# Optimization experiments

Measured on AMD Instinct MI355X. Metric: run time of the kernel, lower is better.

## Reference

```python
import jax, jax.numpy as jnp
import numpy as np


def setup_inputs() -> dict:
    key = jax.random.key(0)
    k1, k2 = jax.random.split(key)
    N, M, Q, D = 4096, 128, 64, 128
    a_embeddings = jax.random.normal(k1, (N, D), dtype=jnp.float32)
    b_embedding_sets = jax.random.normal(k2, (M, Q, D), dtype=jnp.float32)
    gaussian_variance = jnp.full((1,), 0.5, dtype=jnp.float32)  # nn.Parameter default
    return {
        "a_embeddings": a_embeddings,
        "b_embedding_sets": b_embedding_sets,
        "gaussian_variance": gaussian_variance,
    }


def reference(a_embeddings, b_embedding_sets, gaussian_variance):
    # Covariance = var * I, so inv(cov) = I / var and the Mahalanobis term is
    # ||a - mu||^2 / var. Expand the squared distance to avoid the NxMxQxD
    # broadcast intermediate the torch code materializes (same math).
    inv_var = 1.0 / gaussian_variance[0]
    a2 = jnp.sum(a_embeddings * a_embeddings, axis=-1)          # [N]
    b2 = jnp.sum(b_embedding_sets * b_embedding_sets, axis=-1)  # [M, Q]
    ab = jnp.einsum("nd,mqd->nmq", a_embeddings, b_embedding_sets)  # [N, M, Q]
    x2 = (a2[:, None, None] - 2.0 * ab + b2[None, :, :]) * inv_var  # [N, M, Q]
    densities = jnp.exp(-0.5 * x2)                  # [N, M, Q]
    dens_per_cluster = densities.sum(axis=2)        # [N, M]
    prob = dens_per_cluster / (dens_per_cluster.sum(axis=1, keepdims=True) + 1e-10)
    return prob
```

## Files before the change

kernel.cpp:

```cpp
#include <hip/hip_runtime.h>
#include <hip/hip_bf16.h>
#include <math.h>

#define NN 4096
#define MM 128
#define QQ 64
#define DD 128
#define CC (MM * QQ)

typedef short bf16x8 __attribute__((ext_vector_type(8)));
typedef float f32x4  __attribute__((ext_vector_type(4)));

static __device__ inline unsigned short f2bf(float f) {
    __hip_bfloat16 h = __float2bfloat16(f);
    return *reinterpret_cast<unsigned short*>(&h);
}

__global__ __launch_bounds__(256)
void prep_kernel(const float* __restrict__ A, const float* __restrict__ B,
                 unsigned short* __restrict__ Abf, unsigned short* __restrict__ Bbf,
                 float* __restrict__ a2, float* __restrict__ b2)
{
    const int row  = blockIdx.x * 4 + (threadIdx.x >> 6);
    const int lane = threadIdx.x & 63;
    const float* src;
    unsigned short* dst;
    float* nrm;
    if (row < NN) { src = A + (size_t)row * DD; dst = Abf + (size_t)row * DD; nrm = a2 + row; }
    else {
        int r = row - NN;
        src = B + (size_t)r * DD; dst = Bbf + (size_t)r * DD; nrm = b2 + r;
    }
    float2 v = ((const float2*)src)[lane];
    ushort2 u; u.x = f2bf(v.x); u.y = f2bf(v.y);
    ((ushort2*)dst)[lane] = u;
    float s = v.x * v.x + v.y * v.y;
    #pragma unroll
    for (int off = 32; off > 0; off >>= 1) s += __shfl_down(s, off);
    if (lane == 0) *nrm = s;
}

__global__ __launch_bounds__(256, 2)
void kde_mfma_kernel(const unsigned short* __restrict__ Abf,
                     const unsigned short* __restrict__ Bbf,
                     const float* __restrict__ var,
                     const float* __restrict__ a2w,
                     const float* __restrict__ b2w,
                     float* __restrict__ dpc)
{
    __shared__ unsigned short Tile[256 * DD];
    __shared__ float a2s[128];
    __shared__ float b2s[128];

    const int lin = blockIdx.x;
    const int xcd = lin & 7;
    const int loc = lin >> 3;
    const int by  = (xcd << 3) | (loc >> 5);
    const int bx  = loc & 31;
    const int n0  = bx * 128;
    const int c0  = by * 128;

    const int t    = threadIdx.x;
    const int w    = t >> 6;
    const int lane = t & 63;

    const unsigned short* Ab = Abf + (size_t)n0 * DD;
    const unsigned short* Bb = Bbf + (size_t)c0 * DD;
    #pragma unroll
    for (int i = 0; i < 16; ++i) {
        const int slot = w * 1024 + i * 64 + lane;
        const int r    = slot >> 4;
        const int cb   = slot & 15;
        const int scb  = cb ^ (r & 7);
        const unsigned short* g = (r < 128) ? (Ab + r * DD + scb * 8)
                                            : (Bb + (r - 128) * DD + scb * 8);
        unsigned short* lbase = &Tile[(w * 1024 + i * 64) * 8];
        __builtin_amdgcn_global_load_lds(
            (const __attribute__((address_space(1))) unsigned int*)g,
            (__attribute__((address_space(3))) unsigned int*)lbase,
            16, 0, 0);
    }
    if (t < 128)            a2s[t]       = a2w[n0 + t];
    else                    b2s[t - 128] = b2w[c0 + (t - 128)];
    __syncthreads();

    const int l15   = lane & 15;
    const int q     = lane >> 4;
    const int rbase = (w >> 1) * 64;
    const int cbase = (w & 1) * 64;
    const int xr    = l15 & 7;

    f32x4 acc[4][4] = {};
    #pragma unroll
    for (int ks = 0; ks < 4; ++ks) {
        const int off = ((ks * 4 + q) ^ xr) * 8;
        bf16x8 af[4], bf[4];
        #pragma unroll
        for (int i = 0; i < 4; ++i)
            af[i] = *(const bf16x8*)&Tile[(rbase + i * 16 + l15) * DD + off];
        #pragma unroll
        for (int j = 0; j < 4; ++j)
            bf[j] = *(const bf16x8*)&Tile[(128 + cbase + j * 16 + l15) * DD + off];
        #pragma unroll
        for (int i = 0; i < 4; ++i)
            #pragma unroll
            for (int j = 0; j < 4; ++j)
                acc[i][j] = __builtin_amdgcn_mfma_f32_16x16x32_bf16(
                                af[i], bf[j], acc[i][j], 0, 0, 0);
    }

    const float hinv = 0.5f / var[0];
    float rowsum[4][4];
    #pragma unroll
    for (int i = 0; i < 4; ++i) {
        #pragma unroll
        for (int reg = 0; reg < 4; ++reg) {
            const float a2 = a2s[rbase + i * 16 + q * 4 + reg];
            float p = 0.f;
            #pragma unroll
            for (int j = 0; j < 4; ++j) {
                const float b2 = b2s[cbase + j * 16 + l15];
                p += __expf((2.f * acc[i][j][reg] - a2 - b2) * hinv);
            }
            rowsum[i][reg] = p;
        }
    }
    #pragma unroll
    for (int mask = 1; mask < 16; mask <<= 1)
        #pragma unroll
        for (int i = 0; i < 4; ++i)
            #pragma unroll
            for (int reg = 0; reg < 4; ++reg)
                rowsum[i][reg] += __shfl_xor(rowsum[i][reg], mask, 64);

    const int m = (by << 1) + (w & 1);
    if (l15 < 4) {
        const int i = l15;
        #pragma unroll
        for (int reg = 0; reg < 4; ++reg) {
            const int gn = n0 + rbase + i * 16 + q * 4 + reg;
            dpc[(size_t)gn * MM + m] = rowsum[i][reg];
        }
    }
}

__global__ __launch_bounds__(128)
void kde_norm_kernel(float* __restrict__ out)
{
    const int n = blockIdx.x;
    const int t = threadIdx.x;
    const float v = out[(size_t)n * MM + t];
    float s = v;
    #pragma unroll
    for (int off = 32; off > 0; off >>= 1) s += __shfl_down(s, off);
    __shared__ float wsum[2];
    if ((t & 63) == 0) wsum[t >> 6] = s;
    __syncthreads();
    const float tot = wsum[0] + wsum[1];
    out[(size_t)n * MM + t] = v / (tot + 1e-10f);
}

extern "C" void kernel_launch(void* const* d_in, const int* in_sizes, int n_in,
                              void* d_out, int out_size, void* d_ws, size_t ws_size,
                              hipStream_t stream) {
    const float* A   = (const float*)d_in[0];
    const float* B   = (const float*)d_in[1];
    const float* var = (const float*)d_in[2];
    float* out = (float*)d_out;

    unsigned short* Abf = (unsigned short*)d_ws;
    unsigned short* Bbf = Abf + (size_t)NN * DD;
    float* a2 = (float*)(Bbf + (size_t)CC * DD);
    float* b2 = a2 + NN;

    prep_kernel<<<(NN + CC) / 4, 256, 0, stream>>>(A, B, Abf, Bbf, a2, b2);
    kde_mfma_kernel<<<2048, 256, 0, stream>>>(Abf, Bbf, var, a2, b2, out);
    kde_norm_kernel<<<NN, 128, 0, stream>>>(out);
}
```

Measured before the change: 89.44 us.

## Shrink MFMA tile to one cluster per block and reduce row sums via LDS

```diff
diff --git a/kernel.cpp b/kernel.cpp
--- a/kernel.cpp
+++ b/kernel.cpp
@@ -40,7 +40,7 @@
     if (lane == 0) *nrm = s;
 }
 
-__global__ __launch_bounds__(256, 2)
+__global__ __launch_bounds__(256, 3)
 void kde_mfma_kernel(const unsigned short* __restrict__ Abf,
                      const unsigned short* __restrict__ Bbf,
                      const float* __restrict__ var,
@@ -48,17 +48,17 @@
                      const float* __restrict__ b2w,
                      float* __restrict__ dpc)
 {
-    __shared__ unsigned short Tile[256 * DD];
+    __shared__ unsigned short Tile[192 * DD];
     __shared__ float a2s[128];
-    __shared__ float b2s[128];
+    __shared__ float b2s[64];
 
     const int lin = blockIdx.x;
     const int xcd = lin & 7;
     const int loc = lin >> 3;
-    const int by  = (xcd << 3) | (loc >> 5);
+    const int m   = (xcd << 4) | (loc >> 5);
     const int bx  = loc & 31;
     const int n0  = bx * 128;
-    const int c0  = by * 128;
+    const int c0  = m * QQ;
 
     const int t    = threadIdx.x;
     const int w    = t >> 6;
@@ -67,89 +67,84 @@
     const unsigned short* Ab = Abf + (size_t)n0 * DD;
     const unsigned short* Bb = Bbf + (size_t)c0 * DD;
     #pragma unroll
-    for (int i = 0; i < 16; ++i) {
-        const int slot = w * 1024 + i * 64 + lane;
+    for (int i = 0; i < 12; ++i) {
+        const int slot = w * 768 + i * 64 + lane;
         const int r    = slot >> 4;
         const int cb   = slot & 15;
         const int scb  = cb ^ (r & 7);
         const unsigned short* g = (r < 128) ? (Ab + r * DD + scb * 8)
                                             : (Bb + (r - 128) * DD + scb * 8);
-        unsigned short* lbase = &Tile[(w * 1024 + i * 64) * 8];
+        unsigned short* lbase = &Tile[(w * 768 + i * 64) * 8];
         __builtin_amdgcn_global_load_lds(
             (const __attribute__((address_space(1))) unsigned int*)g,
             (__attribute__((address_space(3))) unsigned int*)lbase,
             16, 0, 0);
     }
     if (t < 128)            a2s[t]       = a2w[n0 + t];
-    else                    b2s[t - 128] = b2w[c0 + (t - 128)];
+    else if (t < 192)       b2s[t - 128] = b2w[c0 + (t - 128)];
     __syncthreads();
 
     const int l15   = lane & 15;
     const int q     = lane >> 4;
-    const int rbase = (w >> 1) * 64;
-    const int cbase = (w & 1) * 64;
     const int xr    = l15 & 7;
+    const int rbase = w * 32;
 
-    f32x4 acc[4][4] = {};
+    f32x4 acc[2][4] = {};
     #pragma unroll
     for (int ks = 0; ks < 4; ++ks) {
         const int off = ((ks * 4 + q) ^ xr) * 8;
-        bf16x8 af[4], bf[4];
+        bf16x8 af[2], bf[4];
         #pragma unroll
-        for (int i = 0; i < 4; ++i)
-            af[i] = *(const bf16x8*)&Tile[(rbase + i * 16 + l15) * DD + off];
+        for (int i2 = 0; i2 < 2; ++i2)
+            af[i2] = *(const bf16x8*)&Tile[(rbase + i2 * 16 + l15) * DD + off];
         #pragma unroll
         for (int j = 0; j < 4; ++j)
-            bf[j] = *(const bf16x8*)&Tile[(128 + cbase + j * 16 + l15) * DD + off];
+            bf[j] = *(const bf16x8*)&Tile[(128 + j * 16 + l15) * DD + off];
         #pragma unroll
-        for (int i = 0; i < 4; ++i)
+        for (int i2 = 0; i2 < 2; ++i2)
             #pragma unroll
             for (int j = 0; j < 4; ++j)
-                acc[i][j] = __builtin_amdgcn_mfma_f32_16x16x32_bf16(
-                                af[i], bf[j], acc[i][j], 0, 0, 0);
+                acc[i2][j] = __builtin_amdgcn_mfma_f32_16x16x32_bf16(
+                                 af[i2], bf[j], acc[i2][j], 0, 0, 0);
     }
 
     const float hinv = 0.5f / var[0];
-    float rowsum[4][4];
+    float* S = (float*)&Tile[rbase * DD];
     #pragma unroll
-    for (int i = 0; i < 4; ++i) {
+    for (int i2 = 0; i2 < 2; ++i2) {
         #pragma unroll
         for (int reg = 0; reg < 4; ++reg) {
-            const float a2 = a2s[rbase + i * 16 + q * 4 + reg];
+            const int ri = i2 * 16 + q * 4 + reg;
+            const float a2 = a2s[rbase + ri];
             float p = 0.f;
             #pragma unroll
             for (int j = 0; j < 4; ++j) {
-                const float b2 = b2s[cbase + j * 16 + l15];
-                p += __expf((2.f * acc[i][j][reg] - a2 - b2) * hinv);
+                const float b2 = b2s[j * 16 + l15];
+                p += __expf((2.f * acc[i2][j][reg] - a2 - b2) * hinv);
             }
-            rowsum[i][reg] = p;
+            S[ri * 20 + l15] = p;
         }
     }
-    #pragma unroll
-    for (int mask = 1; mask < 16; mask <<= 1)
-        #pragma unroll
-        for (int i = 0; i < 4; ++i)
-            #pragma unroll
-            for (int reg = 0; reg < 4; ++reg)
-                rowsum[i][reg] += __shfl_xor(rowsum[i][reg], mask, 64);
+    __syncthreads();
 
-    const int m = (by << 1) + (w & 1);
-    if (l15 < 4) {
-        const int i = l15;
-        #pragma unroll
-        for (int reg = 0; reg < 4; ++reg) {
-            const int gn = n0 + rbase + i * 16 + q * 4 + reg;
-            dpc[(size_t)gn * MM + m] = rowsum[i][reg];
-        }
+    if (lane < 32) {
+        const float* Sr = S + lane * 20;
+        f32x4 s0 = *(const f32x4*)&Sr[0];
+        f32x4 s1 = *(const f32x4*)&Sr[4];
+        f32x4 s2 = *(const f32x4*)&Sr[8];
+        f32x4 s3 = *(const f32x4*)&Sr[12];
+        f32x4 ss = s0 + s1 + s2 + s3;
+        const float dens = ss[0] + ss[1] + ss[2] + ss[3];
+        dpc[(size_t)m * NN + n0 + rbase + lane] = dens;
     }
 }
 
 __global__ __launch_bounds__(128)
-void kde_norm_kernel(float* __restrict__ out)
+void kde_norm_kernel(const float* __restrict__ dpc, float* __restrict__ out)
 {
     const int n = blockIdx.x;
     const int t = threadIdx.x;
-    const float v = out[(size_t)n * MM + t];
+    const float v = dpc[(size_t)t * NN + n];
     float s = v;
     #pragma unroll
     for (int off = 32; off > 0; off >>= 1) s += __shfl_down(s, off);
@@ -170,10 +165,11 @@
 
     unsigned short* Abf = (unsigned short*)d_ws;
     unsigned short* Bbf = Abf + (size_t)NN * DD;
-    float* a2 = (float*)(Bbf + (size_t)CC * DD);
-    float* b2 = a2 + NN;
+    float* a2  = (float*)(Bbf + (size_t)CC * DD);
+    float* b2  = a2 + NN;
+    float* dpc = b2 + CC;
 
     prep_kernel<<<(NN + CC) / 4, 256, 0, stream>>>(A, B, Abf, Bbf, a2, b2);
-    kde_mfma_kernel<<<2048, 256, 0, stream>>>(Abf, Bbf, var, a2, b2, out);
-    kde_norm_kernel<<<NN, 128, 0, stream>>>(out);
+    kde_mfma_kernel<<<4096, 256, 0, stream>>>(Abf, Bbf, var, a2, b2, dpc);
+    kde_norm_kernel<<<NN, 128, 0, stream>>>(dpc, out);
 }
```

New measurement: 90.37 us. No clear change (+1.0%).

## Fuse KDE matmul, exp-sum and normalization into one row-block kernel

Applied to the files above, without the earlier changes.

```diff
diff --git a/kernel.cpp b/kernel.cpp
--- a/kernel.cpp
+++ b/kernel.cpp
@@ -40,124 +40,122 @@
     if (lane == 0) *nrm = s;
 }
 
-__global__ __launch_bounds__(256, 2)
-void kde_mfma_kernel(const unsigned short* __restrict__ Abf,
-                     const unsigned short* __restrict__ Bbf,
-                     const float* __restrict__ var,
-                     const float* __restrict__ a2w,
-                     const float* __restrict__ b2w,
-                     float* __restrict__ dpc)
+__global__ __launch_bounds__(1024, 4)
+void kde_fused_kernel(const unsigned short* __restrict__ Abf,
+                      const unsigned short* __restrict__ Bbf,
+                      const float* __restrict__ var,
+                      const float* __restrict__ a2w,
+                      const float* __restrict__ b2w,
+                      float* __restrict__ out)
 {
-    __shared__ unsigned short Tile[256 * DD];
-    __shared__ float a2s[128];
-    __shared__ float b2s[128];
-
-    const int lin = blockIdx.x;
-    const int xcd = lin & 7;
-    const int loc = lin >> 3;
-    const int by  = (xcd << 3) | (loc >> 5);
-    const int bx  = loc & 31;
-    const int n0  = bx * 128;
-    const int c0  = by * 128;
+    __shared__ float tab[16][132];
+    __shared__ float denom[16];
 
     const int t    = threadIdx.x;
     const int w    = t >> 6;
     const int lane = t & 63;
+    const int l15  = lane & 15;
+    const int q    = lane >> 4;
+    const int n0   = blockIdx.x * 16;
+    const int cw0  = w * 512;
+    const int mstart = blockIdx.x & 7;
 
-    const unsigned short* Ab = Abf + (size_t)n0 * DD;
-    const unsigned short* Bb = Bbf + (size_t)c0 * DD;
+    bf16x8 af[4];
+    const unsigned short* Arow = Abf + (size_t)(n0 + l15) * DD;
     #pragma unroll
-    for (int i = 0; i < 16; ++i) {
-        const int slot = w * 1024 + i * 64 + lane;
-        const int r    = slot >> 4;
-        const int cb   = slot & 15;
-        const int scb  = cb ^ (r & 7);
-        const unsigned short* g = (r < 128) ? (Ab + r * DD + scb * 8)
-                                            : (Bb + (r - 128) * DD + scb * 8);
-        unsigned short* lbase = &Tile[(w * 1024 + i * 64) * 8];
-        __builtin_amdgcn_global_load_lds(
-            (const __attribute__((address_space(1))) unsigned int*)g,
-            (__attribute__((address_space(3))) unsigned int*)lbase,
-            16, 0, 0);
+    for (int ks = 0; ks < 4; ++ks)
+        af[ks] = *(const bf16x8*)&Arow[ks * 32 + q * 8];
+
+    float a2v[4];
+    #pragma unroll
+    for (int r = 0; r < 4; ++r) a2v[r] = a2w[n0 + q * 4 + r];
+
+    const float hinv = 0.5f / var[0];
+
+    bf16x8 bb[2][2][4];
+    float  b2r[2][2];
+
+    #define CHUNK_OF(p, cip) ((((mstart + ((p) >> 1)) & 7) << 2) + (((p) & 1) << 1) + (cip))
+
+    #define LOADPAIR(p, ring)                                                   \
+        {                                                                       \
+            _Pragma("unroll")                                                   \
+            for (int cip = 0; cip < 2; ++cip) {                                 \
+                const int cb = cw0 + CHUNK_OF(p, cip) * 16;                     \
+                const unsigned short* Brow = Bbf + (size_t)(cb + l15) * DD;     \
+                _Pragma("unroll")                                               \
+                for (int ks = 0; ks < 4; ++ks)                                  \
+                    bb[ring][cip][ks] = *(const bf16x8*)&Brow[ks * 32 + q * 8]; \
+                b2r[ring][cip] = b2w[cb + l15];                                 \
+            }                                                                   \
+        }
+
+    float dens_part[4] = {0.f, 0.f, 0.f, 0.f};
+
+    #define COMPUTEPAIR(p, ring)                                                \
+        {                                                                       \
+            _Pragma("unroll")                                                   \
+            for (int cip = 0; cip < 2; ++cip) {                                 \
+                f32x4 acc = {0.f, 0.f, 0.f, 0.f};                               \
+                _Pragma("unroll")                                               \
+                for (int ks = 0; ks < 4; ++ks)                                  \
+                    acc = __builtin_amdgcn_mfma_f32_16x16x32_bf16(              \
+                              af[ks], bb[ring][cip][ks], acc, 0, 0, 0);         \
+                const float b2c = b2r[ring][cip];                               \
+                _Pragma("unroll")                                               \
+                for (int r = 0; r < 4; ++r)                                     \
+                    dens_part[r] += __expf((2.f * acc[r] - a2v[r] - b2c) * hinv); \
+            }                                                                   \
+            if (((p) & 1) == 1) {   \
+                _Pragma("unroll")                                               \
+                for (int mask = 1; mask < 16; mask <<= 1)                       \
+                    _Pragma("unroll")                                           \
+                    for (int r = 0; r < 4; ++r)                                 \
+                        dens_part[r] += __shfl_xor(dens_part[r], mask, 64);     \
+                if (l15 == 0) {                                                 \
+                    const int m = (w << 3) + ((mstart + ((p) >> 1)) & 7);       \
+                    _Pragma("unroll")                                           \
+                    for (int r = 0; r < 4; ++r)                                 \
+                        tab[q * 4 + r][m] = dens_part[r];                       \
+                }                                                               \
+                _Pragma("unroll")                                               \
+                for (int r = 0; r < 4; ++r) dens_part[r] = 0.f;                 \
+            }                                                                   \
+        }
+
+    LOADPAIR(0, 0);
+    for (int p = 0; p < 16; p += 2) {
+        if (p + 1 < 16) LOADPAIR(p + 1, 1);
+        COMPUTEPAIR(p, 0);
+        if (p + 2 < 16) LOADPAIR(p + 2, 0);
+        COMPUTEPAIR(p + 1, 1);
     }
-    if (t < 128)            a2s[t]       = a2w[n0 + t];
-    else                    b2s[t - 128] = b2w[c0 + (t - 128)];
     __syncthreads();
 
-    const int l15   = lane & 15;
-    const int q     = lane >> 4;
-    const int rbase = (w >> 1) * 64;
-    const int cbase = (w & 1) * 64;
-    const int xr    = l15 & 7;
+    if (t < 256) {
+        const int row = t >> 4;
+        const int j   = t & 15;
+        const f32x4 s0 = *(const f32x4*)&tab[row][j * 8];
+        const f32x4 s1 = *(const f32x4*)&tab[row][j * 8 + 4];
+        f32x4 ss = s0 + s1;
+        float s = ss[0] + ss[1] + ss[2] + ss[3];
+        #pragma unroll
+        for (int mask = 1; mask < 16; mask <<= 1)
+            s += __shfl_xor(s, mask, 64);
+        if (j == 0) denom[row] = s + 1e-10f;
+    }
+    __syncthreads();
 
-    f32x4 acc[4][4] = {};
-    #pragma unroll
-    for (int ks = 0; ks < 4; ++ks) {
-        const int off = ((ks * 4 + q) ^ xr) * 8;
-        bf16x8 af[4], bf[4];
-        #pragma unroll
-        for (int i = 0; i < 4; ++i)
-            af[i] = *(const bf16x8*)&Tile[(rbase + i * 16 + l15) * DD + off];
-        #pragma unroll
-        for (int j = 0; j < 4; ++j)
-            bf[j] = *(const bf16x8*)&Tile[(128 + cbase + j * 16 + l15) * DD + off];
-        #pragma unroll
-        for (int i = 0; i < 4; ++i)
-            #pragma unroll
-            for (int j = 0; j < 4; ++j)
-                acc[i][j] = __builtin_amdgcn_mfma_f32_16x16x32_bf16(
-                                af[i], bf[j], acc[i][j], 0, 0, 0);
+    {
+        const int idx = t * 2;
+        const int row = idx >> 7;
+        const int m   = idx & 127;
+        const float d = denom[row];
+        float2 v;
+        v.x = tab[row][m]     / d;
+        v.y = tab[row][m + 1] / d;
+        *(float2*)&out[(size_t)(n0 + row) * MM + m] = v;
     }
-
-    const float hinv = 0.5f / var[0];
-    float rowsum[4][4];
-    #pragma unroll
-    for (int i = 0; i < 4; ++i) {
-        #pragma unroll
-        for (int reg = 0; reg < 4; ++reg) {
-            const float a2 = a2s[rbase + i * 16 + q * 4 + reg];
-            float p = 0.f;
-            #pragma unroll
-            for (int j = 0; j < 4; ++j) {
-                const float b2 = b2s[cbase + j * 16 + l15];
-                p += __expf((2.f * acc[i][j][reg] - a2 - b2) * hinv);
-            }
-            rowsum[i][reg] = p;
-        }
-    }
-    #pragma unroll
-    for (int mask = 1; mask < 16; mask <<= 1)
-        #pragma unroll
-        for (int i = 0; i < 4; ++i)
-            #pragma unroll
-            for (int reg = 0; reg < 4; ++reg)
-                rowsum[i][reg] += __shfl_xor(rowsum[i][reg], mask, 64);
-
-    const int m = (by << 1) + (w & 1);
-    if (l15 < 4) {
-        const int i = l15;
-        #pragma unroll
-        for (int reg = 0; reg < 4; ++reg) {
-            const int gn = n0 + rbase + i * 16 + q * 4 + reg;
-            dpc[(size_t)gn * MM + m] = rowsum[i][reg];
-        }
-    }
-}
-
-__global__ __launch_bounds__(128)
-void kde_norm_kernel(float* __restrict__ out)
-{
-    const int n = blockIdx.x;
-    const int t = threadIdx.x;
-    const float v = out[(size_t)n * MM + t];
-    float s = v;
-    #pragma unroll
-    for (int off = 32; off > 0; off >>= 1) s += __shfl_down(s, off);
-    __shared__ float wsum[2];
-    if ((t & 63) == 0) wsum[t >> 6] = s;
-    __syncthreads();
-    const float tot = wsum[0] + wsum[1];
-    out[(size_t)n * MM + t] = v / (tot + 1e-10f);
 }
 
 extern "C" void kernel_launch(void* const* d_in, const int* in_sizes, int n_in,
@@ -174,6 +172,5 @@
     float* b2 = a2 + NN;
 
     prep_kernel<<<(NN + CC) / 4, 256, 0, stream>>>(A, B, Abf, Bbf, a2, b2);
-    kde_mfma_kernel<<<2048, 256, 0, stream>>>(Abf, Bbf, var, a2, b2, out);
-    kde_norm_kernel<<<NN, 128, 0, stream>>>(out);
+    kde_fused_kernel<<<NN / 16, 1024, 0, stream>>>(Abf, Bbf, var, a2, b2, out);
 }
```

New measurement: 127.2 us. 42.3% more time.

## Use 512-thread MFMA blocks, transposed partial-sum layout, and tiled normalization kernel

Applied to the files above, without the earlier changes.

```diff
diff --git a/kernel.cpp b/kernel.cpp
--- a/kernel.cpp
+++ b/kernel.cpp
@@ -21,8 +21,8 @@
                  unsigned short* __restrict__ Abf, unsigned short* __restrict__ Bbf,
                  float* __restrict__ a2, float* __restrict__ b2)
 {
-    const int row  = blockIdx.x * 4 + (threadIdx.x >> 6);
-    const int lane = threadIdx.x & 63;
+    const int row = blockIdx.x * 8 + (threadIdx.x >> 5);
+    const int l32 = threadIdx.x & 31;
     const float* src;
     unsigned short* dst;
     float* nrm;
@@ -31,16 +31,17 @@
         int r = row - NN;
         src = B + (size_t)r * DD; dst = Bbf + (size_t)r * DD; nrm = b2 + r;
     }
-    float2 v = ((const float2*)src)[lane];
-    ushort2 u; u.x = f2bf(v.x); u.y = f2bf(v.y);
-    ((ushort2*)dst)[lane] = u;
-    float s = v.x * v.x + v.y * v.y;
-    #pragma unroll
-    for (int off = 32; off > 0; off >>= 1) s += __shfl_down(s, off);
-    if (lane == 0) *nrm = s;
-}
-
-__global__ __launch_bounds__(256, 2)
+    float4 v = ((const float4*)src)[l32];
+    ushort4 u;
+    u.x = f2bf(v.x); u.y = f2bf(v.y); u.z = f2bf(v.z); u.w = f2bf(v.w);
+    ((ushort4*)dst)[l32] = u;
+    float s = v.x * v.x + v.y * v.y + v.z * v.z + v.w * v.w;
+    #pragma unroll
+    for (int m = 16; m > 0; m >>= 1) s += __shfl_xor(s, m, 64);
+    if (l32 == 0) *nrm = s;
+}
+
+__global__ __launch_bounds__(512, 4)
 void kde_mfma_kernel(const unsigned short* __restrict__ Abf,
                      const unsigned short* __restrict__ Bbf,
                      const float* __restrict__ var,
@@ -51,14 +52,15 @@
     __shared__ unsigned short Tile[256 * DD];
     __shared__ float a2s[128];
     __shared__ float b2s[128];
+    __shared__ float red[8][32];
 
     const int lin = blockIdx.x;
     const int xcd = lin & 7;
     const int loc = lin >> 3;
-    const int by  = (xcd << 3) | (loc >> 5);
-    const int bx  = loc & 31;
-    const int n0  = bx * 128;
-    const int c0  = by * 128;
+    const int cb  = (xcd << 3) | (loc & 7);
+    const int nb  = loc >> 3;
+    const int n0  = nb * 128;
+    const int c0  = cb * 128;
 
     const int t    = threadIdx.x;
     const int w    = t >> 6;
@@ -67,42 +69,42 @@
     const unsigned short* Ab = Abf + (size_t)n0 * DD;
     const unsigned short* Bb = Bbf + (size_t)c0 * DD;
     #pragma unroll
-    for (int i = 0; i < 16; ++i) {
-        const int slot = w * 1024 + i * 64 + lane;
+    for (int i = 0; i < 8; ++i) {
+        const int slot = w * 512 + i * 64 + lane;
         const int r    = slot >> 4;
-        const int cb   = slot & 15;
-        const int scb  = cb ^ (r & 7);
+        const int c16  = slot & 15;
+        const int scb  = c16 ^ (r & 7);
         const unsigned short* g = (r < 128) ? (Ab + r * DD + scb * 8)
                                             : (Bb + (r - 128) * DD + scb * 8);
-        unsigned short* lbase = &Tile[(w * 1024 + i * 64) * 8];
+        unsigned short* lbase = &Tile[(w * 512 + i * 64) * 8];
         __builtin_amdgcn_global_load_lds(
             (const __attribute__((address_space(1))) unsigned int*)g,
             (__attribute__((address_space(3))) unsigned int*)lbase,
             16, 0, 0);
     }
     if (t < 128)            a2s[t]       = a2w[n0 + t];
-    else                    b2s[t - 128] = b2w[c0 + (t - 128)];
+    else if (t < 256)       b2s[t - 128] = b2w[c0 + (t - 128)];
     __syncthreads();
 
     const int l15   = lane & 15;
     const int q     = lane >> 4;
-    const int rbase = (w >> 1) * 64;
-    const int cbase = (w & 1) * 64;
     const int xr    = l15 & 7;
-
-    f32x4 acc[4][4] = {};
+    const int rbase = (w & 3) * 32;
+    const int cbase = (w >> 2) * 64;
+
+    f32x4 acc[2][4] = {};
     #pragma unroll
     for (int ks = 0; ks < 4; ++ks) {
         const int off = ((ks * 4 + q) ^ xr) * 8;
-        bf16x8 af[4], bf[4];
-        #pragma unroll
-        for (int i = 0; i < 4; ++i)
+        bf16x8 af[2], bf[4];
+        #pragma unroll
+        for (int i = 0; i < 2; ++i)
             af[i] = *(const bf16x8*)&Tile[(rbase + i * 16 + l15) * DD + off];
         #pragma unroll
         for (int j = 0; j < 4; ++j)
             bf[j] = *(const bf16x8*)&Tile[(128 + cbase + j * 16 + l15) * DD + off];
         #pragma unroll
-        for (int i = 0; i < 4; ++i)
+        for (int i = 0; i < 2; ++i)
             #pragma unroll
             for (int j = 0; j < 4; ++j)
                 acc[i][j] = __builtin_amdgcn_mfma_f32_16x16x32_bf16(
@@ -110,9 +112,9 @@
     }
 
     const float hinv = 0.5f / var[0];
-    float rowsum[4][4];
-    #pragma unroll
-    for (int i = 0; i < 4; ++i) {
+    float rowsum[2][4];
+    #pragma unroll
+    for (int i = 0; i < 2; ++i) {
         #pragma unroll
         for (int reg = 0; reg < 4; ++reg) {
             const float a2 = a2s[rbase + i * 16 + q * 4 + reg];
@@ -128,36 +130,62 @@
     #pragma unroll
     for (int mask = 1; mask < 16; mask <<= 1)
         #pragma unroll
-        for (int i = 0; i < 4; ++i)
+        for (int i = 0; i < 2; ++i)
             #pragma unroll
             for (int reg = 0; reg < 4; ++reg)
                 rowsum[i][reg] += __shfl_xor(rowsum[i][reg], mask, 64);
 
-    const int m = (by << 1) + (w & 1);
-    if (l15 < 4) {
-        const int i = l15;
-        #pragma unroll
-        for (int reg = 0; reg < 4; ++reg) {
-            const int gn = n0 + rbase + i * 16 + q * 4 + reg;
-            dpc[(size_t)gn * MM + m] = rowsum[i][reg];
-        }
-    }
-}
-
-__global__ __launch_bounds__(128)
-void kde_norm_kernel(float* __restrict__ out)
+    if (l15 == 0) {
+        #pragma unroll
+        for (int i = 0; i < 2; ++i)
+            #pragma unroll
+            for (int reg = 0; reg < 4; ++reg)
+                red[w][i * 16 + q * 4 + reg] = rowsum[i][reg];
+    }
+    const int m = (cb << 1) + (w >> 2);
+    if (lane < 32)
+        dpc[(size_t)m * NN + n0 + rbase + lane] = red[w][lane];
+}
+
+__global__ __launch_bounds__(1024)
+void kde_norm_kernel(const float* __restrict__ dpc, float* __restrict__ out)
 {
-    const int n = blockIdx.x;
-    const int t = threadIdx.x;
-    const float v = out[(size_t)n * MM + t];
-    float s = v;
-    #pragma unroll
-    for (int off = 32; off > 0; off >>= 1) s += __shfl_down(s, off);
-    __shared__ float wsum[2];
-    if ((t & 63) == 0) wsum[t >> 6] = s;
+    __shared__ float tile[MM][65];
+    __shared__ float rden[64];
+    const int n0 = blockIdx.x * 64;
+    const int t  = threadIdx.x;
+
+    #pragma unroll
+    for (int it = 0; it < 2; ++it) {
+        const int m  = (t >> 4) + it * 64;
+        const int nc = (t & 15) * 4;
+        float4 v = *(const float4*)&dpc[(size_t)m * NN + n0 + nc];
+        tile[m][nc]     = v.x;
+        tile[m][nc + 1] = v.y;
+        tile[m][nc + 2] = v.z;
+        tile[m][nc + 3] = v.w;
+    }
     __syncthreads();
-    const float tot = wsum[0] + wsum[1];
-    out[(size_t)n * MM + t] = v / (tot + 1e-10f);
+
+    if (t < 64) {
+        float s = 0.f;
+        #pragma unroll 8
+        for (int m = 0; m < MM; ++m) s += tile[m][t];
+        rden[t] = 1.f / (s + 1e-10f);
+    }
+    __syncthreads();
+
+    const int nloc = t >> 4;
+    const int m0   = (t & 15) * 8;
+    const float r  = rden[nloc];
+    float4 o0, o1;
+    o0.x = tile[m0][nloc] * r;     o0.y = tile[m0 + 1][nloc] * r;
+    o0.z = tile[m0 + 2][nloc] * r; o0.w = tile[m0 + 3][nloc] * r;
+    o1.x = tile[m0 + 4][nloc] * r; o1.y = tile[m0 + 5][nloc] * r;
+    o1.z = tile[m0 + 6][nloc] * r; o1.w = tile[m0 + 7][nloc] * r;
+    float* obase = &out[(size_t)(n0 + nloc) * MM + m0];
+    *(float4*)obase       = o0;
+    *(float4*)(obase + 4) = o1;
 }
 
 extern "C" void kernel_launch(void* const* d_in, const int* in_sizes, int n_in,
@@ -170,10 +198,11 @@
 
     unsigned short* Abf = (unsigned short*)d_ws;
     unsigned short* Bbf = Abf + (size_t)NN * DD;
-    float* a2 = (float*)(Bbf + (size_t)CC * DD);
-    float* b2 = a2 + NN;
-
-    prep_kernel<<<(NN + CC) / 4, 256, 0, stream>>>(A, B, Abf, Bbf, a2, b2);
-    kde_mfma_kernel<<<2048, 256, 0, stream>>>(Abf, Bbf, var, a2, b2, out);
-    kde_norm_kernel<<<NN, 128, 0, stream>>>(out);
-}
+    float* a2  = (float*)(Bbf + (size_t)CC * DD);
+    float* b2  = a2 + NN;
+    float* dpc = b2 + CC;
+
+    prep_kernel<<<(NN + CC) / 8, 256, 0, stream>>>(A, B, Abf, Bbf, a2, b2);
+    kde_mfma_kernel<<<2048, 512, 0, stream>>>(Abf, Bbf, var, a2, b2, dpc);
+    kde_norm_kernel<<<NN / 64, 1024, 0, stream>>>(dpc, out);
+}
```

Result: faster. 85.90 us (-4.0%).
